# Kernel tuning notes

Measured on AMD Instinct MI355X. Metric: run time of the kernel, lower is better.

## Reference

```python
import jax, jax.numpy as jnp
import numpy as np

B, S, D, H = 2, 4096, 512, 4  # batch, seq, hidden, broadcast heads (mask shape)
SCALE = np.float32(np.sqrt(D))  # original divides by np.sqrt(self.d)


def setup_inputs() -> dict:
    key = jax.random.key(0)
    ks = jax.random.split(key, 7)
    lim = np.float32(1.0 / np.sqrt(D))  # torch Linear default init range
    return {
        "q": jax.random.normal(ks[0], (B, S, D), dtype=jnp.float32),
        "k": jax.random.normal(ks[1], (B, S, D), dtype=jnp.float32),
        "v": jax.random.normal(ks[2], (B, S, D), dtype=jnp.float32),
        "Wq": jax.random.uniform(ks[3], (D, D), jnp.float32, -lim, lim),
        "bq": jax.random.uniform(ks[4], (D,), jnp.float32, -lim, lim),
        "Wv": jax.random.uniform(ks[5], (D, D), jnp.float32, -lim, lim),
        "bv": jax.random.uniform(ks[6], (D,), jnp.float32, -lim, lim),
    }


def reference(q, k, v, Wq, bq, Wv, bv):
    # Q projection (original only projects q; key/value raw k is used for scores)
    Q = q @ Wq.T + bq                                   # [B,S,D]
    scores = jnp.einsum("bsd,btd->bst", Q, k) / SCALE   # [B,S,S]
    # zero attn_mask of shape [B,H,S,S] broadcasts scores to [B,H,S,S]
    scores = jnp.broadcast_to(scores[:, None, :, :], (B, H, S, S))
    attn = jax.nn.softmax(scores, axis=-1)              # [B,H,S,S]
    V = v @ Wv.T + bv                                   # [B,S,D]
    out = jnp.einsum("bhst,btd->bhsd", attn, V)         # [B,H,S,D]
    return out
```

## Files before the change

kernel.cpp:

```cpp
#include <hip/hip_runtime.h>
#include <math.h>

#define SEQ 4096
#define DIM 512
#define NBATCH 2

typedef __bf16 bf16;
typedef __bf16 bf16x8 __attribute__((ext_vector_type(8)));
typedef __bf16 bf16x4 __attribute__((ext_vector_type(4)));
typedef float  f32x4  __attribute__((ext_vector_type(4)));

#define GLOAD_LDS16(g, l)                                                              \
  __builtin_amdgcn_global_load_lds((__attribute__((address_space(1))) void*)(g),       \
                                   (__attribute__((address_space(3))) void*)(l), 16, 0, 0)

__device__ __forceinline__ void cvt4(const float* __restrict__ s, bf16* __restrict__ d) {
  f32x4 x = *(const f32x4*)s;
  bf16x4 y;
  y[0] = (bf16)x[0]; y[1] = (bf16)x[1]; y[2] = (bf16)x[2]; y[3] = (bf16)x[3];
  *(bf16x4*)d = y;
}

__global__ __launch_bounds__(256)
void cast5(const float* __restrict__ q, const float* __restrict__ k,
           const float* __restrict__ v, const float* __restrict__ Wq,
           const float* __restrict__ Wv,
           bf16* __restrict__ qb, bf16* __restrict__ kb, bf16* __restrict__ vb,
           bf16* __restrict__ wqb, bf16* __restrict__ wvb) {
  const long NQ = (long)NBATCH * SEQ * DIM;
  const long NW = (long)DIM * DIM;
  long tid = blockIdx.x * 256L + threadIdx.x;
  long nth = gridDim.x * 256L;
  for (long i = tid * 4; i < NQ; i += nth * 4) {
    cvt4(q + i, qb + i);
    cvt4(k + i, kb + i);
    cvt4(v + i, vb + i);
  }
  for (long i = tid * 4; i < NW; i += nth * 4) {
    cvt4(Wq + i, wqb + i);
    cvt4(Wv + i, wvb + i);
  }
}

__global__ __launch_bounds__(256)
void zero_f32(float* __restrict__ p, int n) {
  int i = blockIdx.x * 256 + threadIdx.x;
  if (i < n) p[i] = 0.0f;
}

__global__ __launch_bounds__(256, 2)
void gemm_bt(const bf16* __restrict__ A, const bf16* __restrict__ Bt,
             bf16* __restrict__ C, const float* __restrict__ bias,
             float scale, int N, int K,
             long sA, long sB, long sC, int outMode) {
  __shared__ __align__(16) bf16 lA[128 * 32];
  __shared__ __align__(16) bf16 lB[128 * 32];
  const int t = threadIdx.x;
  const int z = blockIdx.z;
  A += z * sA; Bt += z * sB; C += z * sC;
  const long m0 = (long)blockIdx.x * 128;
  const long n0 = (long)blockIdx.y * 128;
  const int l = t & 63, w = t >> 6;
  const int wr = (w >> 1) * 64, wc = (w & 1) * 64;
  const int lr = l & 15, lg = l >> 4;

  const int c0 = t, c1 = t + 256;
  const int r0 = c0 >> 2, kc0 = (c0 & 3) * 8;
  const int r1 = c1 >> 2, kc1 = (c1 & 3) * 8;
  bf16* lA0 = lA + (w * 64) * 8;
  bf16* lA1 = lA + (256 + w * 64) * 8;
  bf16* lB0 = lB + (w * 64) * 8;
  bf16* lB1 = lB + (256 + w * 64) * 8;
  const bf16* gA0 = A + (m0 + r0) * (long)K + kc0;
  const bf16* gA1 = A + (m0 + r1) * (long)K + kc1;
  const bf16* gB0 = Bt + (n0 + r0) * (long)K + kc0;
  const bf16* gB1 = Bt + (n0 + r1) * (long)K + kc1;

  f32x4 acc[4][4] = {};
  for (int kk = 0; kk < K; kk += 32) {
    GLOAD_LDS16(gA0 + kk, lA0);
    GLOAD_LDS16(gA1 + kk, lA1);
    GLOAD_LDS16(gB0 + kk, lB0);
    GLOAD_LDS16(gB1 + kk, lB1);
    __syncthreads();
    bf16x8 af[4], bfr[4];
#pragma unroll
    for (int m = 0; m < 4; ++m)
      af[m] = *(const bf16x8*)(lA + (wr + m * 16 + lr) * 32 + lg * 8);
#pragma unroll
    for (int n = 0; n < 4; ++n)
      bfr[n] = *(const bf16x8*)(lB + (wc + n * 16 + lr) * 32 + lg * 8);
#pragma unroll
    for (int m = 0; m < 4; ++m)
#pragma unroll
      for (int n = 0; n < 4; ++n)
        acc[m][n] = __builtin_amdgcn_mfma_f32_16x16x32_bf16(af[m], bfr[n], acc[m][n], 0, 0, 0);
    __syncthreads();
  }

#pragma unroll
  for (int n = 0; n < 4; ++n) {
    const long col = n0 + wc + n * 16 + lr;
    const float bcol = bias ? bias[col] : 0.0f;
#pragma unroll
    for (int m = 0; m < 4; ++m) {
      const long rowb = m0 + wr + m * 16 + lg * 4;
#pragma unroll
      for (int r = 0; r < 4; ++r) {
        float vv = (acc[m][n][r] + bcol) * scale;
        bf16 o = (bf16)vv;
        if (outMode == 0) {
          C[(rowb + r) * (long)N + col] = o;
        } else {
          long gr = rowb + r;
          long bb = gr >> 12, ss = gr & 4095;
          C[bb * (long)(DIM * SEQ) + col * (long)SEQ + ss] = o;
        }
      }
    }
  }
}

template <int BI>
__device__ __forceinline__
void stage64(const bf16* const (&gA)[4], const bf16* const (&gB)[BI],
             long kk, bf16* __restrict__ dA, bf16* __restrict__ dB, int w) {
#pragma unroll
  for (int i = 0; i < 4; ++i) GLOAD_LDS16(gA[i] + kk, dA + (i * 256 + w * 64) * 8);
#pragma unroll
  for (int i = 0; i < BI; ++i) GLOAD_LDS16(gB[i] + kk, dB + (i * 256 + w * 64) * 8);
}

template <int NFR>
__device__ __forceinline__
void compute64(const bf16* __restrict__ bufA, const bf16* __restrict__ bufB,
               const int (&offA)[4][2], const int (&offB)[NFR][2],
               f32x4 (&acc)[4][NFR]) {
#pragma unroll
  for (int ks = 0; ks < 2; ++ks) {
    bf16x8 af[4], bfn[NFR];
#pragma unroll
    for (int m = 0; m < 4; ++m) af[m] = *(const bf16x8*)(bufA + offA[m][ks]);
#pragma unroll
    for (int n = 0; n < NFR; ++n) bfn[n] = *(const bf16x8*)(bufB + offB[n][ks]);
#pragma unroll
    for (int m = 0; m < 4; ++m)
#pragma unroll
      for (int n = 0; n < NFR; ++n)
        acc[m][n] = __builtin_amdgcn_mfma_f32_16x16x32_bf16(af[m], bfn[n], acc[m][n], 0, 0, 0);
  }
}

template <int BN, int OUT, int DBUF>
__global__ __launch_bounds__(256, 2)
void gemm64(const bf16* __restrict__ A, const bf16* __restrict__ Bt,
            void* __restrict__ Cv, float* __restrict__ rowsum,
            float scale, int N, int K, long sA, long sB, long sC) {
  constexpr int NFR = BN / 32;
  constexpr int BI = BN / 32;
  __shared__ __align__(16) bf16 lA[1 + DBUF][128 * 64];
  __shared__ __align__(16) bf16 lB[1 + DBUF][BN * 64];
  const int t = threadIdx.x;
  const int z = blockIdx.z;
  A += z * sA; Bt += z * sB;
  const long m0 = (long)blockIdx.x * 128;
  const long n0 = (long)blockIdx.y * BN;
  const int l = t & 63, w = t >> 6;
  const int wr = (w >> 1) * 64, wc = (w & 1) * (BN / 2);
  const int lr = l & 15, lg = l >> 4;

  const bf16* gA[4];
  const bf16* gB[BI];
#pragma unroll
  for (int i = 0; i < 4; ++i) {
    int s = i * 256 + t, row = s >> 3, kc = (s & 7) ^ (row & 7);
    gA[i] = A + (m0 + row) * (long)K + kc * 8;
  }
#pragma unroll
  for (int i = 0; i < BI; ++i) {
    int s = i * 256 + t, row = s >> 3, kc = (s & 7) ^ (row & 7);
    gB[i] = Bt + (n0 + row) * (long)K + kc * 8;
  }

  int offA[4][2], offB[NFR][2];
#pragma unroll
  for (int m = 0; m < 4; ++m)
#pragma unroll
    for (int ks = 0; ks < 2; ++ks)
      offA[m][ks] = (wr + m * 16 + lr) * 64 + (((ks * 4 + lg) ^ (lr & 7)) * 8);
#pragma unroll
  for (int n = 0; n < NFR; ++n)
#pragma unroll
    for (int ks = 0; ks < 2; ++ks)
      offB[n][ks] = (wc + n * 16 + lr) * 64 + (((ks * 4 + lg) ^ (lr & 7)) * 8);

  f32x4 acc[4][NFR] = {};

  if constexpr (DBUF) {
    stage64<BI>(gA, gB, 0, lA[0], lB[0], w);
    __syncthreads();
    for (long kk = 0; kk < K; kk += 128) {
      stage64<BI>(gA, gB, kk + 64, lA[1], lB[1], w);
      compute64<NFR>(lA[0], lB[0], offA, offB, acc);
      __syncthreads();
      if (kk + 128 < K) stage64<BI>(gA, gB, kk + 128, lA[0], lB[0], w);
      compute64<NFR>(lA[1], lB[1], offA, offB, acc);
      __syncthreads();
    }
  } else {
    for (long kk = 0; kk < K; kk += 64) {
      stage64<BI>(gA, gB, kk, lA[0], lB[0], w);
      __syncthreads();
      compute64<NFR>(lA[0], lB[0], offA, offB, acc);
      __syncthreads();
    }
  }

  if constexpr (OUT == 1) {
    bf16* C = (bf16*)Cv + z * sC;
#pragma unroll
    for (int m = 0; m < 4; ++m) {
      const long rowb = m0 + wr + m * 16 + lg * 4;
#pragma unroll
      for (int r = 0; r < 4; ++r) {
        float rsum = 0.0f;
#pragma unroll
        for (int n = 0; n < NFR; ++n) {
          const long col = n0 + wc + n * 16 + lr;
          float e = __expf(acc[m][n][r] * scale);
          bf16 eb = (bf16)e;
          C[(rowb + r) * (long)N + col] = eb;
          rsum += (float)eb;
        }
        rsum += __shfl_xor(rsum, 1);
        rsum += __shfl_xor(rsum, 2);
        rsum += __shfl_xor(rsum, 4);
        rsum += __shfl_xor(rsum, 8);
        if (lr == 0) atomicAdd(rowsum + (long)z * SEQ + rowb + r, rsum);
      }
    }
  } else {
    float* o = (float*)Cv + z * sC;
#pragma unroll
    for (int m = 0; m < 4; ++m) {
      const long rowb = m0 + wr + m * 16 + lg * 4;
#pragma unroll
      for (int r = 0; r < 4; ++r) {
        const float inv = 1.0f / rowsum[(long)z * SEQ + rowb + r];
#pragma unroll
        for (int n = 0; n < NFR; ++n) {
          const long col = n0 + wc + n * 16 + lr;
          float vv = acc[m][n][r] * inv;
          float* p = o + (rowb + r) * (long)DIM + col;
          p[0] = vv;
          p[1L * SEQ * DIM] = vv;
          p[2L * SEQ * DIM] = vv;
          p[3L * SEQ * DIM] = vv;
        }
      }
    }
  }
}

extern "C" void kernel_launch(void* const* d_in, const int* in_sizes, int n_in,
                              void* d_out, int out_size, void* d_ws, size_t ws_size,
                              hipStream_t stream) {
  const float* q  = (const float*)d_in[0];
  const float* k  = (const float*)d_in[1];
  const float* v  = (const float*)d_in[2];
  const float* Wq = (const float*)d_in[3];
  const float* bq = (const float*)d_in[4];
  const float* Wv = (const float*)d_in[5];
  const float* bv = (const float*)d_in[6];
  float* outp = (float*)d_out;

  const long NQ = (long)NBATCH * SEQ * DIM;
  const long NW = (long)DIM * DIM;
  bf16* Qbf = (bf16*)d_ws;
  bf16* Kbf = Qbf + NQ;
  bf16* Vt  = Kbf + NQ;
  bf16* Wqb = Vt + NQ;
  bf16* Wvb = Wqb + NW;
  bf16* Sbuf = Wvb + NW;
  const size_t baseBytes = (size_t)((char*)Sbuf - (char*)d_ws);
  const bool batched = ws_size >= baseBytes + 2ULL * SEQ * SEQ * 2;
  bf16* qb = Sbuf;
  bf16* vb = Sbuf + NQ;
  float* rowsum = (float*)Wqb;

  const float QSCALE = 0.04419417382415922f;

  cast5<<<dim3(2048), dim3(256), 0, stream>>>(q, k, v, Wq, Wv, qb, Kbf, vb, Wqb, Wvb);
  gemm_bt<<<dim3(64, 4, 1), dim3(256), 0, stream>>>(qb, Wqb, Qbf, bq, QSCALE,
                                                    512, 512, 0, 0, 0, 0);
  gemm_bt<<<dim3(64, 4, 1), dim3(256), 0, stream>>>(vb, Wvb, Vt, bv, 1.0f,
                                                    512, 512, 0, 0, 0, 1);
  const long sQK = (long)SEQ * DIM;
  const long sS  = (long)SEQ * SEQ;
  const long sO  = 4L * SEQ * DIM;
  if (batched) {
    zero_f32<<<dim3(32), dim3(256), 0, stream>>>(rowsum, NBATCH * SEQ);
    gemm64<128, 1, 0><<<dim3(32, 32, 2), dim3(256), 0, stream>>>(
        Qbf, Kbf, Sbuf, rowsum, 1.0f, 4096, 512, sQK, sQK, sS);
    gemm64<64, 2, 1><<<dim3(32, 8, 2), dim3(256), 0, stream>>>(
        Sbuf, Vt, outp, rowsum, 1.0f, 512, 4096, sS, sQK, sO);
  } else {
    for (int b = 0; b < 2; ++b) {
      zero_f32<<<dim3(16), dim3(256), 0, stream>>>(rowsum, SEQ);
      gemm64<128, 1, 0><<<dim3(32, 32, 1), dim3(256), 0, stream>>>(
          Qbf + b * sQK, Kbf + b * sQK, Sbuf, rowsum, 1.0f, 4096, 512, 0, 0, 0);
      gemm64<64, 2, 1><<<dim3(32, 8, 1), dim3(256), 0, stream>>>(
          Sbuf, Vt + b * sQK, outp + b * sO, rowsum, 1.0f, 512, 4096, 0, 0, 0);
    }
  }
}
```

Baseline: 256.1 us.

## Unify GEMMs into 512-thread 256x128 tile kernel with prefetch pipeline and swizzle

Replaces the separate projection and attention GEMM kernels with one templated 512-thread kernel using 256x128 tiles. It double-buffers LDS loads two tiles ahead with explicit waitcnt/barriers and setprio, and applies an 8-way workgroup swizzle for L2 locality. The Q and V projections are merged into one launch, and the batch is folded into the M dimension so batched GEMMs run as single-z grids. Larger tiles raise LDS use (96KB per block), which may limit occupancy, and the hand-placed waits depend on exact vmcnt accounting.

```diff
diff --git a/kernel.cpp b/kernel.cpp
--- a/kernel.cpp
+++ b/kernel.cpp
@@ -13,6 +13,10 @@
 #define GLOAD_LDS16(g, l)                                                              \
   __builtin_amdgcn_global_load_lds((__attribute__((address_space(1))) void*)(g),       \
                                    (__attribute__((address_space(3))) void*)(l), 16, 0, 0)
+
+static const long NQ_ = (long)NBATCH * SEQ * DIM;
+static const long NW_ = (long)DIM * DIM;
+#define QSCALE 0.04419417382415922f
 
 __device__ __forceinline__ void cvt4(const float* __restrict__ s, bf16* __restrict__ d) {
   f32x4 x = *(const f32x4*)s;
@@ -27,16 +31,14 @@
            const float* __restrict__ Wv,
            bf16* __restrict__ qb, bf16* __restrict__ kb, bf16* __restrict__ vb,
            bf16* __restrict__ wqb, bf16* __restrict__ wvb) {
-  const long NQ = (long)NBATCH * SEQ * DIM;
-  const long NW = (long)DIM * DIM;
   long tid = blockIdx.x * 256L + threadIdx.x;
   long nth = gridDim.x * 256L;
-  for (long i = tid * 4; i < NQ; i += nth * 4) {
+  for (long i = tid * 4; i < NQ_; i += nth * 4) {
     cvt4(q + i, qb + i);
     cvt4(k + i, kb + i);
     cvt4(v + i, vb + i);
   }
-  for (long i = tid * 4; i < NW; i += nth * 4) {
+  for (long i = tid * 4; i < NW_; i += nth * 4) {
     cvt4(Wq + i, wqb + i);
     cvt4(Wv + i, wvb + i);
   }
@@ -48,186 +50,169 @@
   if (i < n) p[i] = 0.0f;
 }
 
-__global__ __launch_bounds__(256, 2)
-void gemm_bt(const bf16* __restrict__ A, const bf16* __restrict__ Bt,
-             bf16* __restrict__ C, const float* __restrict__ bias,
-             float scale, int N, int K,
-             long sA, long sB, long sC, int outMode) {
-  __shared__ __align__(16) bf16 lA[128 * 32];
-  __shared__ __align__(16) bf16 lB[128 * 32];
+template <int OUT>
+__global__ __launch_bounds__(512, 2)
+void gemm8(const bf16* __restrict__ A, const bf16* __restrict__ Bt,
+           void* __restrict__ Cv, const float* __restrict__ bias0,
+           const float* __restrict__ bias1, float* __restrict__ rowsum,
+           int N, int K, long sB) {
+  __shared__ __align__(16) bf16 lA[2][256 * 64];
+  __shared__ __align__(16) bf16 lB[2][128 * 64];
   const int t = threadIdx.x;
+  const int l = t & 63, w = t >> 6;
+
+  const unsigned bid = blockIdx.y * gridDim.x + blockIdx.x;
+  const unsigned nwg = gridDim.x * gridDim.y;
+  const unsigned q8 = nwg >> 3;
+  const unsigned swz = (bid & 7) * q8 + (bid >> 3);
+  const long m0 = (long)(swz % gridDim.x) * 256;
+  const long n0 = (long)(swz / gridDim.x) * 128;
+
   const int z = blockIdx.z;
-  A += z * sA; Bt += z * sB; C += z * sC;
-  const long m0 = (long)blockIdx.x * 128;
-  const long n0 = (long)blockIdx.y * 128;
-  const int l = t & 63, w = t >> 6;
-  const int wr = (w >> 1) * 64, wc = (w & 1) * 64;
+  if constexpr (OUT == 0) {
+    A += (long)z * NQ_;
+    Bt += (long)z * NW_;
+  } else {
+    Bt += (m0 >> 12) * sB;
+  }
+
+  const int wr = (w >> 1) * 64;
+  const int wc = (w & 1) * 64;
   const int lr = l & 15, lg = l >> 4;
 
-  const int c0 = t, c1 = t + 256;
-  const int r0 = c0 >> 2, kc0 = (c0 & 3) * 8;
-  const int r1 = c1 >> 2, kc1 = (c1 & 3) * 8;
-  bf16* lA0 = lA + (w * 64) * 8;
-  bf16* lA1 = lA + (256 + w * 64) * 8;
-  bf16* lB0 = lB + (w * 64) * 8;
-  bf16* lB1 = lB + (256 + w * 64) * 8;
-  const bf16* gA0 = A + (m0 + r0) * (long)K + kc0;
-  const bf16* gA1 = A + (m0 + r1) * (long)K + kc1;
-  const bf16* gB0 = Bt + (n0 + r0) * (long)K + kc0;
-  const bf16* gB1 = Bt + (n0 + r1) * (long)K + kc1;
+  const bf16* gA[4];
+  const bf16* gB[2];
+#pragma unroll
+  for (int i = 0; i < 4; ++i) {
+    int s = i * 512 + t, row = s >> 3, kc = (s & 7) ^ (row & 7);
+    gA[i] = A + (m0 + row) * (long)K + kc * 8;
+  }
+#pragma unroll
+  for (int i = 0; i < 2; ++i) {
+    int s = i * 512 + t, row = s >> 3, kc = (s & 7) ^ (row & 7);
+    gB[i] = Bt + (n0 + row) * (long)K + kc * 8;
+  }
+
+  int offA[4][2], offB[4][2];
+#pragma unroll
+  for (int m = 0; m < 4; ++m)
+#pragma unroll
+    for (int ks = 0; ks < 2; ++ks)
+      offA[m][ks] = (wr + m * 16 + lr) * 64 + (((ks * 4 + lg) ^ (lr & 7)) * 8);
+#pragma unroll
+  for (int n = 0; n < 4; ++n)
+#pragma unroll
+    for (int ks = 0; ks < 2; ++ks)
+      offB[n][ks] = (wc + n * 16 + lr) * 64 + (((ks * 4 + lg) ^ (lr & 7)) * 8);
+
+  auto stage6 = [&](long koff, bf16* dA, bf16* dB) {
+#pragma unroll
+    for (int i = 0; i < 4; ++i) GLOAD_LDS16(gA[i] + koff, dA + (i * 512 + w * 64) * 8);
+#pragma unroll
+    for (int i = 0; i < 2; ++i) GLOAD_LDS16(gB[i] + koff, dB + (i * 512 + w * 64) * 8);
+  };
 
   f32x4 acc[4][4] = {};
-  for (int kk = 0; kk < K; kk += 32) {
-    GLOAD_LDS16(gA0 + kk, lA0);
-    GLOAD_LDS16(gA1 + kk, lA1);
-    GLOAD_LDS16(gB0 + kk, lB0);
-    GLOAD_LDS16(gB1 + kk, lB1);
-    __syncthreads();
-    bf16x8 af[4], bfr[4];
+  const int NT = K >> 6;
+
+  stage6(0, lA[0], lB[0]);
+  stage6(64, lA[1], lB[1]);
+  asm volatile("s_waitcnt vmcnt(6)" ::: "memory");
+  __builtin_amdgcn_sched_barrier(0);
+  __builtin_amdgcn_s_barrier();
+  __builtin_amdgcn_sched_barrier(0);
+
+  for (int tt = 0; tt < NT; ++tt) {
+    const int cur = tt & 1;
+    const bf16* bufA = lA[cur];
+    const bf16* bufB = lB[cur];
+    bf16x8 a0[4], b0[4];
+#pragma unroll
+    for (int m = 0; m < 4; ++m) a0[m] = *(const bf16x8*)(bufA + offA[m][0]);
+#pragma unroll
+    for (int n = 0; n < 4; ++n) b0[n] = *(const bf16x8*)(bufB + offB[n][0]);
+    asm volatile("s_waitcnt lgkmcnt(0)" ::: "memory");
+    __builtin_amdgcn_sched_barrier(0);
+    __builtin_amdgcn_s_setprio(1);
 #pragma unroll
     for (int m = 0; m < 4; ++m)
-      af[m] = *(const bf16x8*)(lA + (wr + m * 16 + lr) * 32 + lg * 8);
-#pragma unroll
-    for (int n = 0; n < 4; ++n)
-      bfr[n] = *(const bf16x8*)(lB + (wc + n * 16 + lr) * 32 + lg * 8);
+#pragma unroll
+      for (int n = 0; n < 4; ++n)
+        acc[m][n] = __builtin_amdgcn_mfma_f32_16x16x32_bf16(a0[m], b0[n], acc[m][n], 0, 0, 0);
+    __builtin_amdgcn_s_setprio(0);
+    bf16x8 a1[4], b1[4];
+#pragma unroll
+    for (int m = 0; m < 4; ++m) a1[m] = *(const bf16x8*)(bufA + offA[m][1]);
+#pragma unroll
+    for (int n = 0; n < 4; ++n) b1[n] = *(const bf16x8*)(bufB + offB[n][1]);
+    asm volatile("s_waitcnt lgkmcnt(0)" ::: "memory");
+    __builtin_amdgcn_sched_barrier(0);
+    __builtin_amdgcn_s_barrier();
+    __builtin_amdgcn_sched_barrier(0);
+    if (tt + 2 < NT) stage6((long)(tt + 2) * 64, lA[cur], lB[cur]);
+    __builtin_amdgcn_s_setprio(1);
 #pragma unroll
     for (int m = 0; m < 4; ++m)
 #pragma unroll
       for (int n = 0; n < 4; ++n)
-        acc[m][n] = __builtin_amdgcn_mfma_f32_16x16x32_bf16(af[m], bfr[n], acc[m][n], 0, 0, 0);
-    __syncthreads();
-  }
-
-#pragma unroll
-  for (int n = 0; n < 4; ++n) {
-    const long col = n0 + wc + n * 16 + lr;
-    const float bcol = bias ? bias[col] : 0.0f;
+        acc[m][n] = __builtin_amdgcn_mfma_f32_16x16x32_bf16(a1[m], b1[n], acc[m][n], 0, 0, 0);
+    __builtin_amdgcn_s_setprio(0);
+    if (tt + 2 < NT) {
+      asm volatile("s_waitcnt vmcnt(6)" ::: "memory");
+    } else if (tt + 1 < NT) {
+      asm volatile("s_waitcnt vmcnt(0)" ::: "memory");
+    }
+    if (tt + 1 < NT) {
+      __builtin_amdgcn_sched_barrier(0);
+      __builtin_amdgcn_s_barrier();
+      __builtin_amdgcn_sched_barrier(0);
+    }
+  }
+
+  if constexpr (OUT == 0) {
+    if (z == 0) {
+      bf16* C = (bf16*)Cv;
+#pragma unroll
+      for (int n = 0; n < 4; ++n) {
+        const long col = n0 + wc + n * 16 + lr;
+        const float bcol = bias0[col];
+#pragma unroll
+        for (int m = 0; m < 4; ++m) {
+          const long rowb = m0 + wr + m * 16 + lg * 4;
+#pragma unroll
+          for (int r = 0; r < 4; ++r)
+            C[(rowb + r) * (long)DIM + col] = (bf16)((acc[m][n][r] + bcol) * QSCALE);
+        }
+      }
+    } else {
+      bf16* Vt = (bf16*)Cv + NQ_;
+#pragma unroll
+      for (int n = 0; n < 4; ++n) {
+        const long col = n0 + wc + n * 16 + lr;
+        const float bcol = bias1[col];
+#pragma unroll
+        for (int m = 0; m < 4; ++m) {
+          const long rowb = m0 + wr + m * 16 + lg * 4;
+#pragma unroll
+          for (int r = 0; r < 4; ++r) {
+            long gr = rowb + r, bb = gr >> 12, ss = gr & 4095;
+            Vt[bb * (long)(DIM * SEQ) + col * (long)SEQ + ss] = (bf16)(acc[m][n][r] + bcol);
+          }
+        }
+      }
+    }
+  } else if constexpr (OUT == 1) {
+    bf16* C = (bf16*)Cv;
 #pragma unroll
     for (int m = 0; m < 4; ++m) {
       const long rowb = m0 + wr + m * 16 + lg * 4;
 #pragma unroll
       for (int r = 0; r < 4; ++r) {
-        float vv = (acc[m][n][r] + bcol) * scale;
-        bf16 o = (bf16)vv;
-        if (outMode == 0) {
-          C[(rowb + r) * (long)N + col] = o;
-        } else {
-          long gr = rowb + r;
-          long bb = gr >> 12, ss = gr & 4095;
-          C[bb * (long)(DIM * SEQ) + col * (long)SEQ + ss] = o;
-        }
-      }
-    }
-  }
-}
-
-template <int BI>
-__device__ __forceinline__
-void stage64(const bf16* const (&gA)[4], const bf16* const (&gB)[BI],
-             long kk, bf16* __restrict__ dA, bf16* __restrict__ dB, int w) {
-#pragma unroll
-  for (int i = 0; i < 4; ++i) GLOAD_LDS16(gA[i] + kk, dA + (i * 256 + w * 64) * 8);
-#pragma unroll
-  for (int i = 0; i < BI; ++i) GLOAD_LDS16(gB[i] + kk, dB + (i * 256 + w * 64) * 8);
-}
-
-template <int NFR>
-__device__ __forceinline__
-void compute64(const bf16* __restrict__ bufA, const bf16* __restrict__ bufB,
-               const int (&offA)[4][2], const int (&offB)[NFR][2],
-               f32x4 (&acc)[4][NFR]) {
-#pragma unroll
-  for (int ks = 0; ks < 2; ++ks) {
-    bf16x8 af[4], bfn[NFR];
-#pragma unroll
-    for (int m = 0; m < 4; ++m) af[m] = *(const bf16x8*)(bufA + offA[m][ks]);
-#pragma unroll
-    for (int n = 0; n < NFR; ++n) bfn[n] = *(const bf16x8*)(bufB + offB[n][ks]);
-#pragma unroll
-    for (int m = 0; m < 4; ++m)
-#pragma unroll
-      for (int n = 0; n < NFR; ++n)
-        acc[m][n] = __builtin_amdgcn_mfma_f32_16x16x32_bf16(af[m], bfn[n], acc[m][n], 0, 0, 0);
-  }
-}
-
-template <int BN, int OUT, int DBUF>
-__global__ __launch_bounds__(256, 2)
-void gemm64(const bf16* __restrict__ A, const bf16* __restrict__ Bt,
-            void* __restrict__ Cv, float* __restrict__ rowsum,
-            float scale, int N, int K, long sA, long sB, long sC) {
-  constexpr int NFR = BN / 32;
-  constexpr int BI = BN / 32;
-  __shared__ __align__(16) bf16 lA[1 + DBUF][128 * 64];
-  __shared__ __align__(16) bf16 lB[1 + DBUF][BN * 64];
-  const int t = threadIdx.x;
-  const int z = blockIdx.z;
-  A += z * sA; Bt += z * sB;
-  const long m0 = (long)blockIdx.x * 128;
-  const long n0 = (long)blockIdx.y * BN;
-  const int l = t & 63, w = t >> 6;
-  const int wr = (w >> 1) * 64, wc = (w & 1) * (BN / 2);
-  const int lr = l & 15, lg = l >> 4;
-
-  const bf16* gA[4];
-  const bf16* gB[BI];
-#pragma unroll
-  for (int i = 0; i < 4; ++i) {
-    int s = i * 256 + t, row = s >> 3, kc = (s & 7) ^ (row & 7);
-    gA[i] = A + (m0 + row) * (long)K + kc * 8;
-  }
-#pragma unroll
-  for (int i = 0; i < BI; ++i) {
-    int s = i * 256 + t, row = s >> 3, kc = (s & 7) ^ (row & 7);
-    gB[i] = Bt + (n0 + row) * (long)K + kc * 8;
-  }
-
-  int offA[4][2], offB[NFR][2];
-#pragma unroll
-  for (int m = 0; m < 4; ++m)
-#pragma unroll
-    for (int ks = 0; ks < 2; ++ks)
-      offA[m][ks] = (wr + m * 16 + lr) * 64 + (((ks * 4 + lg) ^ (lr & 7)) * 8);
-#pragma unroll
-  for (int n = 0; n < NFR; ++n)
-#pragma unroll
-    for (int ks = 0; ks < 2; ++ks)
-      offB[n][ks] = (wc + n * 16 + lr) * 64 + (((ks * 4 + lg) ^ (lr & 7)) * 8);
-
-  f32x4 acc[4][NFR] = {};
-
-  if constexpr (DBUF) {
-    stage64<BI>(gA, gB, 0, lA[0], lB[0], w);
-    __syncthreads();
-    for (long kk = 0; kk < K; kk += 128) {
-      stage64<BI>(gA, gB, kk + 64, lA[1], lB[1], w);
-      compute64<NFR>(lA[0], lB[0], offA, offB, acc);
-      __syncthreads();
-      if (kk + 128 < K) stage64<BI>(gA, gB, kk + 128, lA[0], lB[0], w);
-      compute64<NFR>(lA[1], lB[1], offA, offB, acc);
-      __syncthreads();
-    }
-  } else {
-    for (long kk = 0; kk < K; kk += 64) {
-      stage64<BI>(gA, gB, kk, lA[0], lB[0], w);
-      __syncthreads();
-      compute64<NFR>(lA[0], lB[0], offA, offB, acc);
-      __syncthreads();
-    }
-  }
-
-  if constexpr (OUT == 1) {
-    bf16* C = (bf16*)Cv + z * sC;
-#pragma unroll
-    for (int m = 0; m < 4; ++m) {
-      const long rowb = m0 + wr + m * 16 + lg * 4;
-#pragma unroll
-      for (int r = 0; r < 4; ++r) {
         float rsum = 0.0f;
 #pragma unroll
-        for (int n = 0; n < NFR; ++n) {
+        for (int n = 0; n < 4; ++n) {
           const long col = n0 + wc + n * 16 + lr;
-          float e = __expf(acc[m][n][r] * scale);
+          float e = __expf(acc[m][n][r]);
           bf16 eb = (bf16)e;
           C[(rowb + r) * (long)N + col] = eb;
           rsum += (float)eb;
@@ -236,26 +221,27 @@
         rsum += __shfl_xor(rsum, 2);
         rsum += __shfl_xor(rsum, 4);
         rsum += __shfl_xor(rsum, 8);
-        if (lr == 0) atomicAdd(rowsum + (long)z * SEQ + rowb + r, rsum);
+        if (lr == 0) atomicAdd(rowsum + rowb + r, rsum);
       }
     }
   } else {
-    float* o = (float*)Cv + z * sC;
+    float* o = (float*)Cv;
 #pragma unroll
     for (int m = 0; m < 4; ++m) {
       const long rowb = m0 + wr + m * 16 + lg * 4;
 #pragma unroll
       for (int r = 0; r < 4; ++r) {
-        const float inv = 1.0f / rowsum[(long)z * SEQ + rowb + r];
-#pragma unroll
-        for (int n = 0; n < NFR; ++n) {
+        const long gr = rowb + r, bb = gr >> 12, ss = gr & 4095;
+        const float inv = 1.0f / rowsum[gr];
+        float* p0 = o + bb * (4L * SEQ * DIM) + ss * (long)DIM;
+#pragma unroll
+        for (int n = 0; n < 4; ++n) {
           const long col = n0 + wc + n * 16 + lr;
           float vv = acc[m][n][r] * inv;
-          float* p = o + (rowb + r) * (long)DIM + col;
-          p[0] = vv;
-          p[1L * SEQ * DIM] = vv;
-          p[2L * SEQ * DIM] = vv;
-          p[3L * SEQ * DIM] = vv;
+          p0[col] = vv;
+          p0[col + 1L * SEQ * DIM] = vv;
+          p0[col + 2L * SEQ * DIM] = vv;
+          p0[col + 3L * SEQ * DIM] = vv;
         }
       }
     }
@@ -274,43 +260,37 @@
   const float* bv = (const float*)d_in[6];
   float* outp = (float*)d_out;
 
-  const long NQ = (long)NBATCH * SEQ * DIM;
-  const long NW = (long)DIM * DIM;
   bf16* Qbf = (bf16*)d_ws;
-  bf16* Kbf = Qbf + NQ;
-  bf16* Vt  = Kbf + NQ;
-  bf16* Wqb = Vt + NQ;
-  bf16* Wvb = Wqb + NW;
-  bf16* Sbuf = Wvb + NW;
+  bf16* Vt  = Qbf + NQ_;
+  bf16* Kbf = Vt + NQ_;
+  bf16* Wqb = Kbf + NQ_;
+  bf16* Wvb = Wqb + NW_;
+  bf16* Sbuf = Wvb + NW_;
   const size_t baseBytes = (size_t)((char*)Sbuf - (char*)d_ws);
   const bool batched = ws_size >= baseBytes + 2ULL * SEQ * SEQ * 2;
   bf16* qb = Sbuf;
-  bf16* vb = Sbuf + NQ;
+  bf16* vb = Sbuf + NQ_;
   float* rowsum = (float*)Wqb;
 
-  const float QSCALE = 0.04419417382415922f;
+  const long sQK = (long)SEQ * DIM;
+  const long sO  = 4L * SEQ * DIM;
 
   cast5<<<dim3(2048), dim3(256), 0, stream>>>(q, k, v, Wq, Wv, qb, Kbf, vb, Wqb, Wvb);
-  gemm_bt<<<dim3(64, 4, 1), dim3(256), 0, stream>>>(qb, Wqb, Qbf, bq, QSCALE,
-                                                    512, 512, 0, 0, 0, 0);
-  gemm_bt<<<dim3(64, 4, 1), dim3(256), 0, stream>>>(vb, Wvb, Vt, bv, 1.0f,
-                                                    512, 512, 0, 0, 0, 1);
-  const long sQK = (long)SEQ * DIM;
-  const long sS  = (long)SEQ * SEQ;
-  const long sO  = 4L * SEQ * DIM;
+  gemm8<0><<<dim3(32, 4, 2), dim3(512), 0, stream>>>(
+      qb, Wqb, Qbf, bq, bv, nullptr, 512, 512, 0);
   if (batched) {
     zero_f32<<<dim3(32), dim3(256), 0, stream>>>(rowsum, NBATCH * SEQ);
-    gemm64<128, 1, 0><<<dim3(32, 32, 2), dim3(256), 0, stream>>>(
-        Qbf, Kbf, Sbuf, rowsum, 1.0f, 4096, 512, sQK, sQK, sS);
-    gemm64<64, 2, 1><<<dim3(32, 8, 2), dim3(256), 0, stream>>>(
-        Sbuf, Vt, outp, rowsum, 1.0f, 512, 4096, sS, sQK, sO);
+    gemm8<1><<<dim3(32, 32, 1), dim3(512), 0, stream>>>(
+        Qbf, Kbf, Sbuf, nullptr, nullptr, rowsum, 4096, 512, sQK);
+    gemm8<2><<<dim3(32, 4, 1), dim3(512), 0, stream>>>(
+        Sbuf, Vt, outp, nullptr, nullptr, rowsum, 512, 4096, sQK);
   } else {
     for (int b = 0; b < 2; ++b) {
       zero_f32<<<dim3(16), dim3(256), 0, stream>>>(rowsum, SEQ);
-      gemm64<128, 1, 0><<<dim3(32, 32, 1), dim3(256), 0, stream>>>(
-          Qbf + b * sQK, Kbf + b * sQK, Sbuf, rowsum, 1.0f, 4096, 512, 0, 0, 0);
-      gemm64<64, 2, 1><<<dim3(32, 8, 1), dim3(256), 0, stream>>>(
-          Sbuf, Vt + b * sQK, outp + b * sO, rowsum, 1.0f, 512, 4096, 0, 0, 0);
-    }
-  }
-}
+      gemm8<1><<<dim3(16, 32, 1), dim3(512), 0, stream>>>(
+          Qbf + b * sQK, Kbf + b * sQK, Sbuf, nullptr, nullptr, rowsum, 4096, 512, sQK);
+      gemm8<2><<<dim3(16, 4, 1), dim3(512), 0, stream>>>(
+          Sbuf, Vt + b * sQK, outp + b * sO, nullptr, nullptr, rowsum, 512, 4096, sQK);
+    }
+  }
+}
```

Measured after the change: 278.1 us. 1.09x slower.
